# Kernel optimization log

Hardware: AMD Instinct MI355X
Metric: run time of the kernel (lower is better)

The kernel has to match this reference:

```python
import jax, jax.numpy as jnp
from jax import lax
import numpy as np

T, K, KEND = 2048, 4, 8
D, H, WD = 100, 256, 300
V, DICT, C = 20000, 700000, 18


def _build_end_indexed(starts, lens, ids, valid):
    # Group gazetteer words by their END position (the step at which the
    # lattice char cell consumes the word memory cell), padded to KEND slots.
    e_ids = np.zeros((T, KEND), np.int32)
    e_start = np.zeros((T, KEND), np.int32)
    e_mask = np.zeros((T, KEND), np.int32)
    cnt = np.zeros(T, np.int64)
    for t in range(T):
        for k in range(K):
            if valid[t, k]:
                e = int(starts[t, k] + lens[t, k] - 1)
                if cnt[e] < KEND:
                    e_ids[e, cnt[e]] = ids[t, k]
                    e_start[e, cnt[e]] = starts[t, k]
                    e_mask[e, cnt[e]] = 1
                    cnt[e] += 1
    return jnp.asarray(e_ids), jnp.asarray(e_start), jnp.asarray(e_mask)


def setup_inputs():
    ks = jax.random.split(jax.random.key(0), 24)
    inputs = jax.random.randint(ks[0], (1, T), 0, V, dtype=jnp.int32)
    rng = np.random.default_rng(0)
    lens = rng.integers(0, 8, size=(T, K))          # word length; valid iff >= 2
    ids = rng.integers(1, DICT, size=(T, K))        # gazetteer word ids
    pos = np.broadcast_to(np.arange(T)[:, None], (T, K))
    # forward direction: word starts at t, ends at t+len-1
    valid_f = (lens >= 2) & (pos + lens - 1 < T)
    fw_ids, fw_start, fw_mask = _build_end_indexed(pos, lens, ids, valid_f)
    # backward direction, expressed in the flipped frame: start' = T-1-(t+len-1)
    starts_b = T - 1 - (pos + lens - 1)
    valid_b = (lens >= 2) & (starts_b >= 0)
    bw_ids, bw_start, bw_mask = _build_end_indexed(starts_b, lens, ids, valid_b)
    s = 0.08
    nrm = lambda k, shape: jax.random.normal(k, shape, jnp.float32) * s
    p = {}
    i = 1
    for pre in ("fw", "bw"):
        p[pre + "_W_ih"] = nrm(ks[i], (D, 3 * H)); i += 1
        p[pre + "_W_hh"] = nrm(ks[i], (H, 3 * H)); i += 1
        p[pre + "_b"] = jnp.zeros((3 * H,), jnp.float32)
        p[pre + "_aW_ih"] = nrm(ks[i], (D, H)); i += 1
        p[pre + "_aW_hh"] = nrm(ks[i], (H, H)); i += 1
        p[pre + "_ab"] = jnp.zeros((H,), jnp.float32)
        p[pre + "_wW_ih"] = nrm(ks[i], (WD, 3 * H)); i += 1
        p[pre + "_wW_hh"] = nrm(ks[i], (H, 3 * H)); i += 1
        p[pre + "_wb"] = jnp.zeros((3 * H,), jnp.float32)
    out = dict(inputs=inputs, fw_ids=fw_ids, fw_start=fw_start, fw_mask=fw_mask,
               bw_ids=bw_ids, bw_start=bw_start, bw_mask=bw_mask, length=T,
               E=nrm(ks[20], (V, D)), word_table=nrm(ks[21], (DICT, WD)),
               W_lin=nrm(ks[22], (2 * H, C)), b_lin=jnp.zeros((C,), jnp.float32))
    out.update(p)
    return out


def _lattice_pass(x, wemb, start, mask, W_ih, W_hh, b, aW_ih, aW_hh, ab, wW_ih, wW_hh, wb):
    # x: [T,D]; wemb: [T,KEND,WD]; start/mask: [T,KEND]
    Tn, Hn = x.shape[0], W_hh.shape[0]

    def step(carry, xs):
        h, c, Hh, Ch = carry                        # Hh/Ch: [T,H] history of char states
        t, xt, we_t, st, m = xs
        mf = m.astype(x.dtype)[:, None]             # [KEND,1]
        hs, cs = Hh[st], Ch[st]                     # char state at each word's start pos
        # WordLSTMCell: c^w = sigmoid(f)*c_start + sigmoid(i)*tanh(g)
        wi, wf, wg = jnp.split(we_t @ wW_ih + hs @ wW_hh + wb, 3, axis=-1)
        cw = jax.nn.sigmoid(wf) * cs + jax.nn.sigmoid(wi) * jnp.tanh(wg)
        # MultiInputLSTMCell char gates
        ii, oo, gg = jnp.split(xt @ W_ih + h @ W_hh + b, 3, axis=-1)
        i_s, o_s, g_t = jax.nn.sigmoid(ii), jax.nn.sigmoid(oo), jnp.tanh(gg)
        # extra input gate per word, then exp-normalization over {i, alphas}
        alpha = jax.nn.sigmoid(xt @ aW_ih + cw @ aW_hh + ab)   # [KEND,H]
        e_i = jnp.exp(i_s)                                      # [H]
        e_a = jnp.exp(alpha) * mf                               # masked slots drop out
        c_merge = (e_i * g_t + (e_a * cw).sum(0)) / (e_i + e_a.sum(0))
        c_plain = (1.0 - i_s) * c + i_s * g_t                   # no-word branch (f = 1-i)
        c_new = jnp.where(jnp.any(m > 0), c_merge, c_plain)
        h_new = o_s * jnp.tanh(c_new)
        return (h_new, c_new, Hh.at[t].set(h_new), Ch.at[t].set(c_new)), h_new

    z = lambda *sh: jnp.zeros(sh, x.dtype)
    init = (z(Hn), z(Hn), z(Tn, Hn), z(Tn, Hn))
    _, hseq = lax.scan(step, init, (jnp.arange(Tn), x, wemb, start, mask))
    return hseq                                      # [T,H]


def reference(inputs, fw_ids, fw_start, fw_mask, bw_ids, bw_start, bw_mask, length, E,
              word_table, W_lin, b_lin,
              fw_W_ih, fw_W_hh, fw_b, fw_aW_ih, fw_aW_hh, fw_ab, fw_wW_ih, fw_wW_hh, fw_wb,
              bw_W_ih, bw_W_hh, bw_b, bw_aW_ih, bw_aW_hh, bw_ab, bw_wW_ih, bw_wW_hh, bw_wb):
    x = E[inputs[0]]                                 # [T,D] char embeddings (batch=1)
    hf = _lattice_pass(x, word_table[fw_ids], fw_start, fw_mask,
                       fw_W_ih, fw_W_hh, fw_b, fw_aW_ih, fw_aW_hh, fw_ab,
                       fw_wW_ih, fw_wW_hh, fw_wb)
    hb = _lattice_pass(x[::-1], word_table[bw_ids], bw_start, bw_mask,
                       bw_W_ih, bw_W_hh, bw_b, bw_aW_ih, bw_aW_hh, bw_ab,
                       bw_wW_ih, bw_wW_hh, bw_wb)[::-1]
    return (jnp.concatenate([hf, hb], axis=-1) @ W_lin + b_lin)[None]  # [1,T,C]
```

## Files before the change

kernel.cpp:

```cpp
#include <hip/hip_runtime.h>
#include <hip/hip_bf16.h>


#define TSEQ 2048
#define KEND 8
#define DEMB 100
#define H    256
#define H3   768
#define WD   300
#define CCLS 18
#define NTH  256

typedef __attribute__((ext_vector_type(8))) short bf16x8;
typedef __attribute__((ext_vector_type(4))) float f32x4;

#define LO_AT  0
#define LO_A1  131072
#define LO_VS  131584
#define LO_UR  133120
#define LO_RC  143872
#define LO_A2  152064
#define LO_AWS 156288
#define LO_MT  160384
#define SMEM_SCAN 160640

__device__ __forceinline__ float sigf(float x) { return 1.0f / (1.0f + expf(-x)); }
__device__ __forceinline__ float bf2f(unsigned u) { return __uint_as_float(u << 16); }
__device__ __forceinline__ unsigned f2bf(float f) {
  union { float f; unsigned u; } x; x.f = f;
  unsigned r = x.u + 0x7fffu + ((x.u >> 16) & 1u);
  return r >> 16;
}

__global__ __launch_bounds__(64) void k_pack(
    const float* __restrict__ W_hh_f, const float* __restrict__ wW_hh_f, const float* __restrict__ aW_hh_f,
    const float* __restrict__ W_hh_b, const float* __restrict__ wW_hh_b, const float* __restrict__ aW_hh_b,
    unsigned short* __restrict__ Wpk)
{
  const int T = blockIdx.x, dir = blockIdx.y;
  const int lane = threadIdx.x;
  const float* Wg = dir ? W_hh_b  : W_hh_f;
  const float* Ww = dir ? wW_hh_b : wW_hh_f;
  const float* Wa = dir ? aW_hh_b : aW_hh_f;
  for (int ks = 0; ks < 8; ++ks) {
    bf16x8 sv;
#pragma unroll
    for (int e = 0; e < 8; ++e) {
      const int k = ks * 32 + (lane >> 4) * 8 + e;
      float f;
      if (T < 96) {
        const int c = T * 16 + (lane & 15);
        f = (c < H3) ? Wg[(size_t)k * H3 + c] : Ww[(size_t)k * H3 + (c - H3)];
      } else {
        const int c = (T - 96) * 16 + (lane & 15);
        f = Wa[(size_t)k * H + c];
      }
      sv[e] = (short)f2bf(f);
    }
    *(bf16x8*)(Wpk + (((size_t)dir * 112 + T) * 8 + ks) * 512 + lane * 8) = sv;
  }
}

__global__ __launch_bounds__(256) void k_embed(
    const int* __restrict__ inputs, const float* __restrict__ E,
    const float* __restrict__ W_ih_f, const float* __restrict__ b_f,
    const float* __restrict__ aW_ih_f, const float* __restrict__ ab_f,
    const float* __restrict__ W_ih_b, const float* __restrict__ b_b,
    const float* __restrict__ aW_ih_b, const float* __restrict__ ab_b,
    __hip_bfloat16* __restrict__ xg, float* __restrict__ xa)
{
  const int t = blockIdx.x, dir = blockIdx.y;
  const int tid = threadIdx.x;
  const float* W_ih = dir ? W_ih_b : W_ih_f;
  const float* bb   = dir ? b_b    : b_f;
  const float* aW   = dir ? aW_ih_b : aW_ih_f;
  const float* ab   = dir ? ab_b   : ab_f;
  const int src = dir ? (TSEQ - 1 - t) : t;

  __shared__ float xr[DEMB];
  if (tid < DEMB) xr[tid] = E[(size_t)inputs[src] * DEMB + tid];
  __syncthreads();

  float a0 = bb[tid], a1 = bb[H + tid], a2 = bb[2 * H + tid], a3 = ab[tid];
  for (int r = 0; r < DEMB; r += 4) {
    const float4 e4 = *reinterpret_cast<const float4*>(&xr[r]);
    const float ev[4] = {e4.x, e4.y, e4.z, e4.w};
#pragma unroll
    for (int kk = 0; kk < 4; ++kk) {
      const float* wp = W_ih + (size_t)(r + kk) * H3 + tid;
      a0 += ev[kk] * wp[0];
      a1 += ev[kk] * wp[H];
      a2 += ev[kk] * wp[2 * H];
      a3 += ev[kk] * aW[(size_t)(r + kk) * H + tid];
    }
  }
  __hip_bfloat16* xgrow = xg + ((size_t)dir * TSEQ + t) * H3;
  xgrow[tid]         = __float2bfloat16(a0);
  xgrow[H + tid]     = __float2bfloat16(a1);
  xgrow[2 * H + tid] = __float2bfloat16(a2);
  xa[((size_t)dir * TSEQ + t) * H + tid] = a3;
}

__global__ __launch_bounds__(256) void k_wordgates(
    const int* __restrict__ fw_ids, const int* __restrict__ fw_mask,
    const int* __restrict__ bw_ids, const int* __restrict__ bw_mask,
    const float* __restrict__ word_table,
    const float* __restrict__ wW_ih_f, const float* __restrict__ wb_f,
    const float* __restrict__ wW_ih_b, const float* __restrict__ wb_b,
    __hip_bfloat16* __restrict__ wg)
{
  const int t = blockIdx.x, dir = blockIdx.y;
  const int tid = threadIdx.x;
  const int* ids = (dir ? bw_ids : fw_ids) + t * KEND;
  const int* msk = (dir ? bw_mask : fw_mask) + t * KEND;
  const float* wW = dir ? wW_ih_b : wW_ih_f;
  const float* wb = dir ? wb_b    : wb_f;

  __shared__ float we[KEND][WD];
  for (int w = 0; w < KEND; ++w) {
    if (msk[w]) {
      const float* src = word_table + (size_t)ids[w] * WD;
      for (int i = tid; i < WD; i += 256) we[w][i] = src[i];
    }
  }
  __syncthreads();

  __hip_bfloat16* out = wg + ((size_t)dir * TSEQ + t) * KEND * H3;
  for (int w = 0; w < KEND; ++w) {
    if (!msk[w]) continue;
    float a0 = wb[tid], a1 = wb[H + tid], a2 = wb[2 * H + tid];
    for (int r = 0; r < WD; r += 4) {
      const float4 e4 = *reinterpret_cast<const float4*>(&we[w][r]);
      const float ev[4] = {e4.x, e4.y, e4.z, e4.w};
#pragma unroll
      for (int kk = 0; kk < 4; ++kk) {
        const float* wp = wW + (size_t)(r + kk) * H3 + tid;
        a0 += ev[kk] * wp[0];
        a1 += ev[kk] * wp[H];
        a2 += ev[kk] * wp[2 * H];
      }
    }
    out[w * H3 + tid]         = __float2bfloat16(a0);
    out[w * H3 + H + tid]     = __float2bfloat16(a1);
    out[w * H3 + 2 * H + tid] = __float2bfloat16(a2);
  }
}

__global__ __launch_bounds__(NTH, 1) void k_scan(
    const __hip_bfloat16* __restrict__ xg, const float* __restrict__ xa,
    const __hip_bfloat16* __restrict__ wgG, float* __restrict__ hseq,
    const int* __restrict__ fw_start, const int* __restrict__ fw_mask,
    const int* __restrict__ bw_start, const int* __restrict__ bw_mask,
    const unsigned short* __restrict__ Wpk,
    unsigned long long* __restrict__ xb, unsigned* __restrict__ xf)
{
  const int gid = blockIdx.x;
  if (gid != 0 && gid != 1 && gid != 8 && gid != 9) return;
  const int dir  = gid & 1;
  const int side = gid >> 3;

  extern __shared__ char smem[];
  unsigned short* A1_16 = (unsigned short*)(smem + LO_A1);
  unsigned short* vS16  = (unsigned short*)(smem + LO_VS);
  unsigned short* ur16  = (unsigned short*)(smem + LO_UR);
  float* ringC = (float*)(smem + LO_RC);
  unsigned short* awS16 = (unsigned short*)(smem + LO_AWS);
  int* metaI = (int*)(smem + LO_MT);

  const int tid  = threadIdx.x;
  const int lane = tid & 63;
  const int wv   = tid >> 6;
  const int lmod = lane & 15;
  const int lgrp = lane >> 4;

  const int* startA = dir ? bw_start : fw_start;
  const int* maskA  = dir ? bw_mask  : fw_mask;
  const char* WpkD = (const char*)(Wpk + (size_t)dir * 112 * 8 * 512);

  unsigned long long* myPay = xb + (size_t)((dir * 2 + side) * 2) * 192;
  const unsigned long long* peerPay = xb + (size_t)((dir * 2 + (side ^ 1)) * 2) * 192;
  unsigned* myFlag   = xf + (dir * 2 + side) * 32;
  unsigned* peerFlag = xf + (dir * 2 + (side ^ 1)) * 32;

  bf16x8 rW[12][8];
  {
    const char* rp = WpkD + (size_t)(side * 48 + wv * 12) * 8192 + lane * 16;
#pragma unroll
    for (int n = 0; n < 12; ++n)
#pragma unroll
      for (int ks = 0; ks < 8; ++ks)
        rW[n][ks] = *(const bf16x8*)(rp + (n * 8 + ks) * 1024);
  }
  for (int o = tid * 16; o < 131072; o += NTH * 16)
    *(uint4*)(smem + LO_AT + o) = *(const uint4*)(WpkD + (size_t)96 * 8192 + o);
  if (tid < 32) *(uint4*)(smem + LO_A1 + tid * 16) = uint4{0, 0, 0, 0};
  for (int o = tid * 16; o < 4224; o += NTH * 16)
    *(uint4*)(smem + LO_A2 + o) = uint4{0, 0, 0, 0};
  for (int o = tid * 16; o < 8192; o += NTH * 16)
    *(uint4*)(smem + LO_RC + o) = uint4{0, 0, 0, 0};

  unsigned nxI = 0, nxO = 0, nxG = 0; float nxA = 0.f;
  unsigned cxI = 0, cxO = 0, cxG = 0; float cxA = 0.f;
  int nmt = 0;
  {
    const unsigned short* xr = (const unsigned short*)(xg + (size_t)dir * TSEQ * H3);
    nxI = xr[tid]; nxO = xr[H + tid]; nxG = xr[2 * H + tid];
    nxA = xa[(size_t)dir * TSEQ * H + tid];
    if (wv == 3) {
      if (lane < 8) nmt = maskA[lane];
      else if (lane < 16) nmt = startA[lane - 8];
    }
  }
  __syncthreads();
  if (wv == 3) {
    int mAll[8], sAll[8];
#pragma unroll
    for (int s = 0; s < 8; ++s) { mAll[s] = __shfl(nmt, s); sAll[s] = __shfl(nmt, 8 + s); }
    if (lane == 0) {
      int n = 0;
      for (int s = 0; s < 8; ++s)
        if (mAll[s]) { metaI[1 + n] = s; metaI[9 + n] = sAll[s]; ++n; }
      metaI[0] = n;
    }
  }
  cxI = nxI; cxO = nxO; cxG = nxG; cxA = nxA;
  __syncthreads();

  for (int t = 0; t < TSEQ; ++t) {
    const int par = t & 1;
    const int* mp = metaI + par * 32;
    const int nw = mp[0];
    const int us7 = (t + 6) % 7;
    unsigned short* stage16 = side ? (ur16 + us7 * 768) : vS16;
    unsigned short* rcv16   = side ? vS16 : (ur16 + us7 * 768);
    int hasL2w = 0;
    for (int w = 0; w < nw; ++w) hasL2w |= (mp[9 + w] == t - 1);

    unsigned short wgv[24];
#pragma unroll
    for (int it = 0; it < 8; ++it) {
      const int u0 = tid + it * NTH;
      if (u0 < nw * 256) {
        const int w = u0 >> 8, j = u0 & 255;
        const int slot = mp[1 + w];
        const unsigned short* wgp =
            (const unsigned short*)wgG + ((size_t)(dir * TSEQ + t) * KEND + slot) * H3 + j;
        wgv[it * 3 + 0] = wgp[0];
        wgv[it * 3 + 1] = wgp[256];
        wgv[it * 3 + 2] = wgp[512];
      }
    }

#pragma unroll
    for (int g = 0; g < 2; ++g) {
      f32x4 acc[6];
#pragma unroll
      for (int n = 0; n < 6; ++n) acc[n] = f32x4{0.f, 0.f, 0.f, 0.f};
#pragma unroll
      for (int ks = 0; ks < 8; ++ks) {
        const bf16x8 av = *(const bf16x8*)(smem + LO_A1 + ks * 64 + lgrp * 16);
#pragma unroll
        for (int n = 0; n < 6; ++n)
          acc[n] = __builtin_amdgcn_mfma_f32_16x16x32_bf16(av, rW[g * 6 + n][ks], acc[n], 0, 0, 0);
      }
      if (lane < 16) {
#pragma unroll
        for (int n = 0; n < 6; ++n)
          stage16[(wv * 12 + g * 6 + n) * 16 + lane] = (unsigned short)f2bf(acc[n][0]);
      }
    }
    __syncthreads();

    if (tid < 192) {
      const unsigned long long q = *(const unsigned long long*)((const char*)stage16 + tid * 8);
      __hip_atomic_store(myPay + par * 192 + tid, q, __ATOMIC_RELAXED, __HIP_MEMORY_SCOPE_AGENT);
    }
    __syncthreads();

    if (tid == 0)
      __hip_atomic_store(myFlag, (unsigned)(t + 1), __ATOMIC_RELAXED, __HIP_MEMORY_SCOPE_AGENT);

    {
      const int tn = (t + 1 < TSEQ) ? t + 1 : TSEQ - 1;
      const unsigned short* xr = (const unsigned short*)(xg + ((size_t)dir * TSEQ + tn) * H3);
      nxI = xr[tid]; nxO = xr[H + tid]; nxG = xr[2 * H + tid];
      nxA = xa[((size_t)dir * TSEQ + tn) * H + tid];
      if (wv == 3) {
        if (lane < 8) nmt = maskA[tn * KEND + lane];
        else if (lane < 16) nmt = startA[tn * KEND + (lane - 8)];
      }
    }
#pragma unroll
    for (int it = 0; it < 8; ++it) {
      const int u0 = tid + it * NTH;
      if (u0 < nw * 256) {
        const int w = u0 >> 8, j = u0 & 255;
        const int s = mp[9 + w];
        if (side == 1 || s != t - 1) {
          const unsigned short* ur = ur16 + (s % 7) * 768;
          const float wi  = bf2f(wgv[it * 3 + 0]) + bf2f(ur[j]);
          const float wf  = bf2f(wgv[it * 3 + 1]) + bf2f(ur[256 + j]);
          const float wgg = bf2f(wgv[it * 3 + 2]) + bf2f(ur[512 + j]);
          const float cs  = ringC[(s & 7) * 256 + j];
          const float cv  = sigf(wf) * cs + sigf(wi) * tanhf(wgg);
          *(unsigned short*)(smem + LO_A2 + w * 528 + j * 2) = (unsigned short)f2bf(cv);
        }
      }
    }

    if (tid == 0) {
      while (__hip_atomic_load(peerFlag, __ATOMIC_RELAXED, __HIP_MEMORY_SCOPE_AGENT) < (unsigned)(t + 1))
        __builtin_amdgcn_s_sleep(1);
    }
    __syncthreads();

    if (tid < 192) {
      const unsigned long long q =
          __hip_atomic_load(peerPay + par * 192 + tid, __ATOMIC_RELAXED, __HIP_MEMORY_SCOPE_AGENT);
      *(unsigned long long*)((char*)rcv16 + tid * 8) = q;
    }
    __syncthreads();

    if (hasL2w) {
      if (side == 0) {
#pragma unroll
        for (int it = 0; it < 8; ++it) {
          const int u0 = tid + it * NTH;
          if (u0 < nw * 256) {
            const int w = u0 >> 8, j = u0 & 255;
            const int s = mp[9 + w];
            if (s == t - 1) {
              const unsigned short* ur = ur16 + (s % 7) * 768;
              const float wi  = bf2f(wgv[it * 3 + 0]) + bf2f(ur[j]);
              const float wf  = bf2f(wgv[it * 3 + 1]) + bf2f(ur[256 + j]);
              const float wgg = bf2f(wgv[it * 3 + 2]) + bf2f(ur[512 + j]);
              const float cs  = ringC[(s & 7) * 256 + j];
              const float cv  = sigf(wf) * cs + sigf(wi) * tanhf(wgg);
              *(unsigned short*)(smem + LO_A2 + w * 528 + j * 2) = (unsigned short)f2bf(cv);
            }
          }
        }
      }
      __syncthreads();
    }

    if (nw > 0) {
      const int r2 = (lmod > 7) ? 7 : lmod;
      f32x4 ac[4];
#pragma unroll
      for (int m = 0; m < 4; ++m) ac[m] = f32x4{0.f, 0.f, 0.f, 0.f};
#pragma unroll
      for (int ks = 0; ks < 8; ++ks) {
        const bf16x8 a2v = *(const bf16x8*)(smem + LO_A2 + r2 * 528 + ks * 64 + lgrp * 16);
#pragma unroll
        for (int m = 0; m < 4; ++m) {
          const bf16x8 b = *(const bf16x8*)(smem + LO_AT + (size_t)(wv * 4 + m) * 8192 + ks * 1024 + lane * 16);
          ac[m] = __builtin_amdgcn_mfma_f32_16x16x32_bf16(a2v, b, ac[m], 0, 0, 0);
        }
      }
#pragma unroll
      for (int m = 0; m < 4; ++m) {
#pragma unroll
        for (int r = 0; r < 4; ++r) {
          const int row = lgrp * 4 + r;
          if (row < nw) awS16[row * 256 + (wv * 4 + m) * 16 + lmod] = (unsigned short)f2bf(ac[m][r]);
        }
      }
    }
    __syncthreads();

    {
      const int j = tid;
      const float i_s = sigf(bf2f(cxI) + bf2f(vS16[j]));
      const float o_s = sigf(bf2f(cxO) + bf2f(vS16[256 + j]));
      const float g_t = tanhf(bf2f(cxG) + bf2f(vS16[512 + j]));
      float cnew;
      if (nw > 0) {
        const float e_i = expf(i_s);
        float num = e_i * g_t, den = e_i;
        for (int w = 0; w < nw; ++w) {
          const float a  = sigf(cxA + bf2f(awS16[w * 256 + j]));
          const float ea = expf(a);
          num += ea * bf2f(*(const unsigned short*)(smem + LO_A2 + w * 528 + j * 2));
          den += ea;
        }
        cnew = num / den;
      } else {
        cnew = (1.f - i_s) * ringC[((t - 1) & 7) * 256 + j] + i_s * g_t;
      }
      const float hnew = o_s * tanhf(cnew);
      ringC[(t & 7) * 256 + j] = cnew;
      A1_16[j] = (unsigned short)f2bf(hnew);
      if ((side == 0) == (j < 128))
        hseq[((size_t)dir * TSEQ + t) * H + j] = hnew;
    }
    if (wv == 3) {
      int mAll[8], sAll[8];
#pragma unroll
      for (int s = 0; s < 8; ++s) { mAll[s] = __shfl(nmt, s); sAll[s] = __shfl(nmt, 8 + s); }
      if (lane == 0) {
        int* mq = metaI + ((t + 1) & 1) * 32;
        int n = 0;
        for (int s = 0; s < 8; ++s)
          if (mAll[s]) { mq[1 + n] = s; mq[9 + n] = sAll[s]; ++n; }
        mq[0] = n;
      }
    }
    cxI = nxI; cxO = nxO; cxG = nxG; cxA = nxA;
    __syncthreads();
  }
}

__global__ __launch_bounds__(64) void k_proj(
    const float* __restrict__ hseq, const float* __restrict__ W_lin,
    const float* __restrict__ b_lin, float* __restrict__ out)
{
  const int t = blockIdx.x;
  const int tid = threadIdx.x;
  __shared__ float hrow[2 * H];
  for (int i = tid; i < H; i += 64) {
    hrow[i]     = hseq[(size_t)t * H + i];
    hrow[H + i] = hseq[((size_t)TSEQ + (TSEQ - 1 - t)) * H + i];
  }
  __syncthreads();
  if (tid < CCLS) {
    float acc = b_lin[tid];
    for (int j = 0; j < 2 * H; ++j) acc += hrow[j] * W_lin[(size_t)j * CCLS + tid];
    out[(size_t)t * CCLS + tid] = acc;
  }
}

extern "C" void kernel_launch(void* const* d_in, const int* in_sizes, int n_in,
                              void* d_out, int out_size, void* d_ws, size_t ws_size,
                              hipStream_t stream)
{
  const int* inputs   = (const int*)d_in[0];
  const int* fw_ids   = (const int*)d_in[1];
  const int* fw_start = (const int*)d_in[2];
  const int* fw_mask  = (const int*)d_in[3];
  const int* bw_ids   = (const int*)d_in[4];
  const int* bw_start = (const int*)d_in[5];
  const int* bw_mask  = (const int*)d_in[6];
  const float* E          = (const float*)d_in[8];
  const float* word_table = (const float*)d_in[9];
  const float* W_lin      = (const float*)d_in[10];
  const float* b_lin      = (const float*)d_in[11];
  const float* fw_W_ih  = (const float*)d_in[12];
  const float* fw_W_hh  = (const float*)d_in[13];
  const float* fw_b     = (const float*)d_in[14];
  const float* fw_aW_ih = (const float*)d_in[15];
  const float* fw_aW_hh = (const float*)d_in[16];
  const float* fw_ab    = (const float*)d_in[17];
  const float* fw_wW_ih = (const float*)d_in[18];
  const float* fw_wW_hh = (const float*)d_in[19];
  const float* fw_wb    = (const float*)d_in[20];
  const float* bw_W_ih  = (const float*)d_in[21];
  const float* bw_W_hh  = (const float*)d_in[22];
  const float* bw_b     = (const float*)d_in[23];
  const float* bw_aW_ih = (const float*)d_in[24];
  const float* bw_aW_hh = (const float*)d_in[25];
  const float* bw_ab    = (const float*)d_in[26];
  const float* bw_wW_ih = (const float*)d_in[27];
  const float* bw_wW_hh = (const float*)d_in[28];
  const float* bw_wb    = (const float*)d_in[29];

  char* p = (char*)d_ws;
  __hip_bfloat16* xg = (__hip_bfloat16*)p;  p += (size_t)2 * TSEQ * H3 * 2;
  float* xa   = (float*)p;                  p += (size_t)2 * TSEQ * H * 4;
  float* hseq = (float*)p;                  p += (size_t)2 * TSEQ * H * 4;
  __hip_bfloat16* wg = (__hip_bfloat16*)p;  p += (size_t)2 * TSEQ * KEND * H3 * 2;
  unsigned short* Wpk = (unsigned short*)p; p += (size_t)2 * 112 * 8 * 512 * 2;
  unsigned long long* xb = (unsigned long long*)p; p += (size_t)2 * 2 * 2 * 192 * 8;
  unsigned* xf = (unsigned*)p;              p += 512;

  hipFuncSetAttribute((const void*)k_scan,
                      hipFuncAttributeMaxDynamicSharedMemorySize, SMEM_SCAN);
  hipMemsetAsync(xf, 0, 512, stream);

  k_pack<<<dim3(112, 2), 64, 0, stream>>>(
      fw_W_hh, fw_wW_hh, fw_aW_hh, bw_W_hh, bw_wW_hh, bw_aW_hh, Wpk);
  k_embed<<<dim3(TSEQ, 2), 256, 0, stream>>>(
      inputs, E, fw_W_ih, fw_b, fw_aW_ih, fw_ab, bw_W_ih, bw_b, bw_aW_ih, bw_ab, xg, xa);
  k_wordgates<<<dim3(TSEQ, 2), 256, 0, stream>>>(
      fw_ids, fw_mask, bw_ids, bw_mask, word_table, fw_wW_ih, fw_wb, bw_wW_ih, bw_wb, wg);
  k_scan<<<16, NTH, SMEM_SCAN, stream>>>(
      xg, xa, wg, hseq, fw_start, fw_mask, bw_start, bw_mask, Wpk, xb, xf);
  k_proj<<<TSEQ, 64, 0, stream>>>(hseq, W_lin, b_lin, (float*)d_out);
}
```

Baseline: 14.28 ms.

## Make side-1 block a pipelined word-recurrence helper with tagged h/u exchange

Previously two blocks per direction did a symmetric step: each computed half the gates, exchanged payloads and waited on a flag every step. Now side 0 computes all char-cell gates locally. Side 1 only waits for h, computes the word-cell recurrent product, and publishes it as timestamp-tagged 64-bit words, so no separate flag is needed. Side 0 reads the word product lazily with a lag of two steps, and waits for the previous step's product only when a word starting at t-1 is present. This takes the peer round trip off the critical path at most steps, but spinning on tagged loads adds polling traffic.

```diff
diff --git a/kernel.cpp b/kernel.cpp
--- a/kernel.cpp
+++ b/kernel.cpp
@@ -16,13 +16,13 @@
 
 #define LO_AT  0
 #define LO_A1  131072
-#define LO_VS  131584
-#define LO_UR  133120
-#define LO_RC  143872
-#define LO_A2  152064
-#define LO_AWS 156288
-#define LO_MT  160384
-#define SMEM_SCAN 160640
+#define LO_UR  131584
+#define LO_RC  142336
+#define LO_PRE 150528
+#define LO_A2  153600
+#define LO_AWS 157824
+#define LO_MT  161920
+#define SMEM_SCAN 162176
 
 __device__ __forceinline__ float sigf(float x) { return 1.0f / (1.0f + expf(-x)); }
 __device__ __forceinline__ float bf2f(unsigned u) { return __uint_as_float(u << 16); }
@@ -152,7 +152,7 @@
     const int* __restrict__ fw_start, const int* __restrict__ fw_mask,
     const int* __restrict__ bw_start, const int* __restrict__ bw_mask,
     const unsigned short* __restrict__ Wpk,
-    unsigned long long* __restrict__ xb, unsigned* __restrict__ xf)
+    unsigned long long* __restrict__ hx, unsigned long long* __restrict__ ux)
 {
   const int gid = blockIdx.x;
   if (gid != 0 && gid != 1 && gid != 8 && gid != 9) return;
@@ -161,9 +161,9 @@
 
   extern __shared__ char smem[];
   unsigned short* A1_16 = (unsigned short*)(smem + LO_A1);
-  unsigned short* vS16  = (unsigned short*)(smem + LO_VS);
   unsigned short* ur16  = (unsigned short*)(smem + LO_UR);
   float* ringC = (float*)(smem + LO_RC);
+  float* preS  = (float*)(smem + LO_PRE);
   unsigned short* awS16 = (unsigned short*)(smem + LO_AWS);
   int* metaI = (int*)(smem + LO_MT);
 
@@ -173,14 +173,10 @@
   const int lmod = lane & 15;
   const int lgrp = lane >> 4;
 
-  const int* startA = dir ? bw_start : fw_start;
-  const int* maskA  = dir ? bw_mask  : fw_mask;
   const char* WpkD = (const char*)(Wpk + (size_t)dir * 112 * 8 * 512);
 
-  unsigned long long* myPay = xb + (size_t)((dir * 2 + side) * 2) * 192;
-  const unsigned long long* peerPay = xb + (size_t)((dir * 2 + (side ^ 1)) * 2) * 192;
-  unsigned* myFlag   = xf + (dir * 2 + side) * 32;
-  unsigned* peerFlag = xf + (dir * 2 + (side ^ 1)) * 32;
+  unsigned long long* hbuf = hx + (size_t)dir * 2 * 128;
+  unsigned long long* ubuf = ux + (size_t)dir * 2 * 384;
 
   bf16x8 rW[12][8];
   {
@@ -191,6 +187,51 @@
       for (int ks = 0; ks < 8; ++ks)
         rW[n][ks] = *(const bf16x8*)(rp + (n * 8 + ks) * 1024);
   }
+
+  if (side == 1) {
+    __syncthreads();
+    for (int t = 1; t < TSEQ; ++t) {
+      if (tid < 128) {
+        const unsigned long long* src = hbuf + (size_t)((t - 1) & 1) * 128;
+        unsigned long long q;
+        do { q = __hip_atomic_load(src + tid, __ATOMIC_RELAXED, __HIP_MEMORY_SCOPE_AGENT); }
+        while ((unsigned)(q >> 32) != (unsigned)t);
+        *(unsigned*)((char*)A1_16 + tid * 4) = (unsigned)q;
+      }
+      __syncthreads();
+#pragma unroll
+      for (int g = 0; g < 2; ++g) {
+        f32x4 acc[6];
+#pragma unroll
+        for (int n = 0; n < 6; ++n) acc[n] = f32x4{0.f, 0.f, 0.f, 0.f};
+#pragma unroll
+        for (int ks = 0; ks < 8; ++ks) {
+          const bf16x8 av = *(const bf16x8*)(smem + LO_A1 + ks * 64 + lgrp * 16);
+#pragma unroll
+          for (int n = 0; n < 6; ++n)
+            acc[n] = __builtin_amdgcn_mfma_f32_16x16x32_bf16(av, rW[g * 6 + n][ks], acc[n], 0, 0, 0);
+        }
+#pragma unroll
+        for (int n = 0; n < 6; ++n) {
+          const unsigned hb = f2bf(acc[n][0]) & 0xffffu;
+          const unsigned ob = (unsigned)__shfl_down((int)hb, 1) & 0xffffu;
+          if (lane < 16 && !(lane & 1)) {
+            const int tix = wv * 12 + g * 6 + n;
+            const unsigned long long q =
+                ((unsigned long long)(unsigned)t << 32) | (hb | (ob << 16));
+            __hip_atomic_store(ubuf + (size_t)((t - 1) & 1) * 384 + tix * 8 + (lane >> 1), q,
+                               __ATOMIC_RELAXED, __HIP_MEMORY_SCOPE_AGENT);
+          }
+        }
+      }
+      __syncthreads();
+    }
+    return;
+  }
+
+  const int* startA = dir ? bw_start : fw_start;
+  const int* maskA  = dir ? bw_mask  : fw_mask;
+
   for (int o = tid * 16; o < 131072; o += NTH * 16)
     *(uint4*)(smem + LO_AT + o) = *(const uint4*)(WpkD + (size_t)96 * 8192 + o);
   if (tid < 32) *(uint4*)(smem + LO_A1 + tid * 16) = uint4{0, 0, 0, 0};
@@ -226,13 +267,12 @@
   cxI = nxI; cxO = nxO; cxG = nxG; cxA = nxA;
   __syncthreads();
 
+  int uHave = -1;
+
   for (int t = 0; t < TSEQ; ++t) {
     const int par = t & 1;
     const int* mp = metaI + par * 32;
     const int nw = mp[0];
-    const int us7 = (t + 6) % 7;
-    unsigned short* stage16 = side ? (ur16 + us7 * 768) : vS16;
-    unsigned short* rcv16   = side ? vS16 : (ur16 + us7 * 768);
     int hasL2w = 0;
     for (int w = 0; w < nw; ++w) hasL2w |= (mp[9 + w] == t - 1);
 
@@ -266,19 +306,24 @@
       if (lane < 16) {
 #pragma unroll
         for (int n = 0; n < 6; ++n)
-          stage16[(wv * 12 + g * 6 + n) * 16 + lane] = (unsigned short)f2bf(acc[n][0]);
-      }
-    }
-    __syncthreads();
-
-    if (tid < 192) {
-      const unsigned long long q = *(const unsigned long long*)((const char*)stage16 + tid * 8);
-      __hip_atomic_store(myPay + par * 192 + tid, q, __ATOMIC_RELAXED, __HIP_MEMORY_SCOPE_AGENT);
-    }
-    __syncthreads();
-
-    if (tid == 0)
-      __hip_atomic_store(myFlag, (unsigned)(t + 1), __ATOMIC_RELAXED, __HIP_MEMORY_SCOPE_AGENT);
+          preS[(wv * 12 + g * 6 + n) * 16 + lane] = acc[n][0];
+      }
+    }
+
+    if (t >= 2 && uHave < t - 2) {
+      const int s = t - 2;
+      const unsigned long long* src = ubuf + (size_t)(s & 1) * 384;
+      unsigned long long q;
+      do { q = __hip_atomic_load(src + tid, __ATOMIC_RELAXED, __HIP_MEMORY_SCOPE_AGENT); }
+      while ((unsigned)(q >> 32) != (unsigned)(s + 1));
+      *(unsigned*)((char*)ur16 + (s % 7) * 1536 + tid * 4) = (unsigned)q;
+      if (tid < 128) {
+        do { q = __hip_atomic_load(src + 256 + tid, __ATOMIC_RELAXED, __HIP_MEMORY_SCOPE_AGENT); }
+        while ((unsigned)(q >> 32) != (unsigned)(s + 1));
+        *(unsigned*)((char*)ur16 + (s % 7) * 1536 + (256 + tid) * 4) = (unsigned)q;
+      }
+      uHave = t - 2;
+    }
 
     {
       const int tn = (t + 1 < TSEQ) ? t + 1 : TSEQ - 1;
@@ -290,13 +335,15 @@
         else if (lane < 16) nmt = startA[tn * KEND + (lane - 8)];
       }
     }
+    __syncthreads();
+
 #pragma unroll
     for (int it = 0; it < 8; ++it) {
       const int u0 = tid + it * NTH;
       if (u0 < nw * 256) {
         const int w = u0 >> 8, j = u0 & 255;
         const int s = mp[9 + w];
-        if (side == 1 || s != t - 1) {
+        if (s != t - 1) {
           const unsigned short* ur = ur16 + (s % 7) * 768;
           const float wi  = bf2f(wgv[it * 3 + 0]) + bf2f(ur[j]);
           const float wf  = bf2f(wgv[it * 3 + 1]) + bf2f(ur[256 + j]);
@@ -307,42 +354,41 @@
         }
       }
     }
-
-    if (tid == 0) {
-      while (__hip_atomic_load(peerFlag, __ATOMIC_RELAXED, __HIP_MEMORY_SCOPE_AGENT) < (unsigned)(t + 1))
-        __builtin_amdgcn_s_sleep(1);
+    if (hasL2w) {
+      {
+        const int s = t - 1;
+        const unsigned long long* src = ubuf + (size_t)(s & 1) * 384;
+        unsigned long long q;
+        do { q = __hip_atomic_load(src + tid, __ATOMIC_RELAXED, __HIP_MEMORY_SCOPE_AGENT); }
+        while ((unsigned)(q >> 32) != (unsigned)(s + 1));
+        *(unsigned*)((char*)ur16 + (s % 7) * 1536 + tid * 4) = (unsigned)q;
+        if (tid < 128) {
+          do { q = __hip_atomic_load(src + 256 + tid, __ATOMIC_RELAXED, __HIP_MEMORY_SCOPE_AGENT); }
+          while ((unsigned)(q >> 32) != (unsigned)(s + 1));
+          *(unsigned*)((char*)ur16 + (s % 7) * 1536 + (256 + tid) * 4) = (unsigned)q;
+        }
+        uHave = t - 1;
+      }
+      __syncthreads();
+#pragma unroll
+      for (int it = 0; it < 8; ++it) {
+        const int u0 = tid + it * NTH;
+        if (u0 < nw * 256) {
+          const int w = u0 >> 8, j = u0 & 255;
+          const int s = mp[9 + w];
+          if (s == t - 1) {
+            const unsigned short* ur = ur16 + (s % 7) * 768;
+            const float wi  = bf2f(wgv[it * 3 + 0]) + bf2f(ur[j]);
+            const float wf  = bf2f(wgv[it * 3 + 1]) + bf2f(ur[256 + j]);
+            const float wgg = bf2f(wgv[it * 3 + 2]) + bf2f(ur[512 + j]);
+            const float cs  = ringC[(s & 7) * 256 + j];
+            const float cv  = sigf(wf) * cs + sigf(wi) * tanhf(wgg);
+            *(unsigned short*)(smem + LO_A2 + w * 528 + j * 2) = (unsigned short)f2bf(cv);
+          }
+        }
+      }
     }
     __syncthreads();
-
-    if (tid < 192) {
-      const unsigned long long q =
-          __hip_atomic_load(peerPay + par * 192 + tid, __ATOMIC_RELAXED, __HIP_MEMORY_SCOPE_AGENT);
-      *(unsigned long long*)((char*)rcv16 + tid * 8) = q;
-    }
-    __syncthreads();
-
-    if (hasL2w) {
-      if (side == 0) {
-#pragma unroll
-        for (int it = 0; it < 8; ++it) {
-          const int u0 = tid + it * NTH;
-          if (u0 < nw * 256) {
-            const int w = u0 >> 8, j = u0 & 255;
-            const int s = mp[9 + w];
-            if (s == t - 1) {
-              const unsigned short* ur = ur16 + (s % 7) * 768;
-              const float wi  = bf2f(wgv[it * 3 + 0]) + bf2f(ur[j]);
-              const float wf  = bf2f(wgv[it * 3 + 1]) + bf2f(ur[256 + j]);
-              const float wgg = bf2f(wgv[it * 3 + 2]) + bf2f(ur[512 + j]);
-              const float cs  = ringC[(s & 7) * 256 + j];
-              const float cv  = sigf(wf) * cs + sigf(wi) * tanhf(wgg);
-              *(unsigned short*)(smem + LO_A2 + w * 528 + j * 2) = (unsigned short)f2bf(cv);
-            }
-          }
-        }
-      }
-      __syncthreads();
-    }
 
     if (nw > 0) {
       const int r2 = (lmod > 7) ? 7 : lmod;
@@ -371,9 +417,9 @@
 
     {
       const int j = tid;
-      const float i_s = sigf(bf2f(cxI) + bf2f(vS16[j]));
-      const float o_s = sigf(bf2f(cxO) + bf2f(vS16[256 + j]));
-      const float g_t = tanhf(bf2f(cxG) + bf2f(vS16[512 + j]));
+      const float i_s = sigf(bf2f(cxI) + preS[j]);
+      const float o_s = sigf(bf2f(cxO) + preS[256 + j]);
+      const float g_t = tanhf(bf2f(cxG) + preS[512 + j]);
       float cnew;
       if (nw > 0) {
         const float e_i = expf(i_s);
@@ -390,9 +436,16 @@
       }
       const float hnew = o_s * tanhf(cnew);
       ringC[(t & 7) * 256 + j] = cnew;
-      A1_16[j] = (unsigned short)f2bf(hnew);
-      if ((side == 0) == (j < 128))
-        hseq[((size_t)dir * TSEQ + t) * H + j] = hnew;
+      const unsigned hb = f2bf(hnew) & 0xffffu;
+      A1_16[j] = (unsigned short)hb;
+      hseq[((size_t)dir * TSEQ + t) * H + j] = hnew;
+      const unsigned ob = (unsigned)__shfl_xor((int)hb, 1) & 0xffffu;
+      if (!(tid & 1)) {
+        const unsigned long long q =
+            ((unsigned long long)(unsigned)(t + 1) << 32) | (hb | (ob << 16));
+        __hip_atomic_store(hbuf + (size_t)par * 128 + (tid >> 1), q,
+                           __ATOMIC_RELAXED, __HIP_MEMORY_SCOPE_AGENT);
+      }
     }
     if (wv == 3) {
       int mAll[8], sAll[8];
@@ -470,12 +523,12 @@
   float* hseq = (float*)p;                  p += (size_t)2 * TSEQ * H * 4;
   __hip_bfloat16* wg = (__hip_bfloat16*)p;  p += (size_t)2 * TSEQ * KEND * H3 * 2;
   unsigned short* Wpk = (unsigned short*)p; p += (size_t)2 * 112 * 8 * 512 * 2;
-  unsigned long long* xb = (unsigned long long*)p; p += (size_t)2 * 2 * 2 * 192 * 8;
-  unsigned* xf = (unsigned*)p;              p += 512;
+  unsigned long long* hx = (unsigned long long*)p; p += (size_t)2 * 2 * 128 * 8;
+  unsigned long long* ux = (unsigned long long*)p; p += (size_t)2 * 2 * 384 * 8;
 
   hipFuncSetAttribute((const void*)k_scan,
                       hipFuncAttributeMaxDynamicSharedMemorySize, SMEM_SCAN);
-  hipMemsetAsync(xf, 0, 512, stream);
+  hipMemsetAsync(hx, 0, (size_t)2 * 2 * 128 * 8 + (size_t)2 * 2 * 384 * 8, stream);
 
   k_pack<<<dim3(112, 2), 64, 0, stream>>>(
       fw_W_hh, fw_wW_hh, fw_aW_hh, bw_W_hh, bw_wW_hh, bw_aW_hh, Wpk);
@@ -484,6 +537,6 @@
   k_wordgates<<<dim3(TSEQ, 2), 256, 0, stream>>>(
       fw_ids, fw_mask, bw_ids, bw_mask, word_table, fw_wW_ih, fw_wb, bw_wW_ih, bw_wb, wg);
   k_scan<<<16, NTH, SMEM_SCAN, stream>>>(
-      xg, xa, wg, hseq, fw_start, fw_mask, bw_start, bw_mask, Wpk, xb, xf);
+      xg, xa, wg, hseq, fw_start, fw_mask, bw_start, bw_mask, Wpk, hx, ux);
   k_proj<<<TSEQ, 64, 0, stream>>>(hseq, W_lin, b_lin, (float*)d_out);
 }
```

Result: slower. 16.33 ms (+14.4%).

## Decouple cross-block exchange and defer word-cell payload waits in lattice scan

Applied to the files above, without the earlier changes.

The symmetric per-step handshake between the two blocks of each direction becomes asymmetric. Side 0 now publishes the char-gate matvec and side 1 waits for it only right before the cell update. Side 1's word-gate payload is consumed lazily by side 0: immediately only when a word started at the previous step, otherwise prefetched at the end of the step. Payload packing moves into registers via lane shuffles with direct atomic stores, which removes two block barriers per step. This is meant to shorten the serial per-step critical path, but the flag and slot parity logic is more delicate and could race or deadlock if wrong.

```diff
diff --git a/kernel.cpp b/kernel.cpp
--- a/kernel.cpp
+++ b/kernel.cpp
@@ -152,7 +152,8 @@
     const int* __restrict__ fw_start, const int* __restrict__ fw_mask,
     const int* __restrict__ bw_start, const int* __restrict__ bw_mask,
     const unsigned short* __restrict__ Wpk,
-    unsigned long long* __restrict__ xb, unsigned* __restrict__ xf)
+    unsigned long long* __restrict__ vb, unsigned long long* __restrict__ ub,
+    unsigned* __restrict__ xf)
 {
   const int gid = blockIdx.x;
   if (gid != 0 && gid != 1 && gid != 8 && gid != 9) return;
@@ -177,10 +178,11 @@
   const int* maskA  = dir ? bw_mask  : fw_mask;
   const char* WpkD = (const char*)(Wpk + (size_t)dir * 112 * 8 * 512);
 
-  unsigned long long* myPay = xb + (size_t)((dir * 2 + side) * 2) * 192;
-  const unsigned long long* peerPay = xb + (size_t)((dir * 2 + (side ^ 1)) * 2) * 192;
-  unsigned* myFlag   = xf + (dir * 2 + side) * 32;
-  unsigned* peerFlag = xf + (dir * 2 + (side ^ 1)) * 32;
+  unsigned long long* myPay = (side ? ub : vb) + (size_t)dir * 2 * 192;
+  const unsigned long long* ubuf = ub + (size_t)dir * 2 * 192;
+  const unsigned long long* vbuf = vb + (size_t)dir * 2 * 192;
+  unsigned* vFlag = xf + dir * 64;
+  unsigned* uFlag = xf + dir * 64 + 32;
 
   bf16x8 rW[12][8];
   {
@@ -226,13 +228,16 @@
   cxI = nxI; cxO = nxO; cxG = nxG; cxA = nxA;
   __syncthreads();
 
+  int uHave = -1, pfValid = 0, pfS = 0;
+  unsigned long long pq = 0;
+
   for (int t = 0; t < TSEQ; ++t) {
     const int par = t & 1;
     const int* mp = metaI + par * 32;
     const int nw = mp[0];
     const int us7 = (t + 6) % 7;
     unsigned short* stage16 = side ? (ur16 + us7 * 768) : vS16;
-    unsigned short* rcv16   = side ? vS16 : (ur16 + us7 * 768);
+    const int pubSlot = side ? (par ^ 1) : par;
     int hasL2w = 0;
     for (int w = 0; w < nw; ++w) hasL2w |= (mp[9 + w] == t - 1);
 
@@ -263,22 +268,32 @@
         for (int n = 0; n < 6; ++n)
           acc[n] = __builtin_amdgcn_mfma_f32_16x16x32_bf16(av, rW[g * 6 + n][ks], acc[n], 0, 0, 0);
       }
-      if (lane < 16) {
-#pragma unroll
-        for (int n = 0; n < 6; ++n)
-          stage16[(wv * 12 + g * 6 + n) * 16 + lane] = (unsigned short)f2bf(acc[n][0]);
-      }
-    }
-    __syncthreads();
-
-    if (tid < 192) {
-      const unsigned long long q = *(const unsigned long long*)((const char*)stage16 + tid * 8);
-      __hip_atomic_store(myPay + par * 192 + tid, q, __ATOMIC_RELAXED, __HIP_MEMORY_SCOPE_AGENT);
-    }
-    __syncthreads();
-
-    if (tid == 0)
-      __hip_atomic_store(myFlag, (unsigned)(t + 1), __ATOMIC_RELAXED, __HIP_MEMORY_SCOPE_AGENT);
+#pragma unroll
+      for (int n = 0; n < 6; ++n) {
+        const unsigned hb = f2bf(acc[n][0]) & 0xffffu;
+        const unsigned v1 = (unsigned)__shfl_down((int)hb, 1) & 0xffffu;
+        const unsigned v2 = (unsigned)__shfl_down((int)hb, 2) & 0xffffu;
+        const unsigned v3 = (unsigned)__shfl_down((int)hb, 3) & 0xffffu;
+        if (lane < 16) {
+          const int tix = wv * 12 + g * 6 + n;
+          stage16[tix * 16 + lane] = (unsigned short)hb;
+          if ((lane & 3) == 0) {
+            const unsigned long long q =
+                (unsigned long long)(hb | (v1 << 16)) |
+                ((unsigned long long)(v2 | (v3 << 16)) << 32);
+            __hip_atomic_store(myPay + (size_t)pubSlot * 192 + tix * 4 + (lane >> 2), q,
+                               __ATOMIC_RELAXED, __HIP_MEMORY_SCOPE_AGENT);
+          }
+        }
+      }
+    }
+
+    if (side == 0 && pfValid) {
+      if (tid < 192)
+        *(unsigned long long*)((char*)ur16 + (pfS % 7) * 1536 + tid * 8) = pq;
+      uHave = pfS;
+      pfValid = 0;
+    }
 
     {
       const int tn = (t + 1 < TSEQ) ? t + 1 : TSEQ - 1;
@@ -290,6 +305,13 @@
         else if (lane < 16) nmt = startA[tn * KEND + (lane - 8)];
       }
     }
+    __syncthreads();
+
+    if (tid == 0) {
+      if (side) __hip_atomic_store(uFlag, (unsigned)t, __ATOMIC_RELAXED, __HIP_MEMORY_SCOPE_AGENT);
+      else      __hip_atomic_store(vFlag, (unsigned)(t + 1), __ATOMIC_RELAXED, __HIP_MEMORY_SCOPE_AGENT);
+    }
+
 #pragma unroll
     for (int it = 0; it < 8; ++it) {
       const int u0 = tid + it * NTH;
@@ -308,66 +330,82 @@
       }
     }
 
-    if (tid == 0) {
-      while (__hip_atomic_load(peerFlag, __ATOMIC_RELAXED, __HIP_MEMORY_SCOPE_AGENT) < (unsigned)(t + 1))
-        __builtin_amdgcn_s_sleep(1);
-    }
-    __syncthreads();
-
-    if (tid < 192) {
-      const unsigned long long q =
-          __hip_atomic_load(peerPay + par * 192 + tid, __ATOMIC_RELAXED, __HIP_MEMORY_SCOPE_AGENT);
-      *(unsigned long long*)((char*)rcv16 + tid * 8) = q;
-    }
-    __syncthreads();
-
-    if (hasL2w) {
-      if (side == 0) {
-#pragma unroll
-        for (int it = 0; it < 8; ++it) {
-          const int u0 = tid + it * NTH;
-          if (u0 < nw * 256) {
-            const int w = u0 >> 8, j = u0 & 255;
-            const int s = mp[9 + w];
-            if (s == t - 1) {
-              const unsigned short* ur = ur16 + (s % 7) * 768;
-              const float wi  = bf2f(wgv[it * 3 + 0]) + bf2f(ur[j]);
-              const float wf  = bf2f(wgv[it * 3 + 1]) + bf2f(ur[256 + j]);
-              const float wgg = bf2f(wgv[it * 3 + 2]) + bf2f(ur[512 + j]);
-              const float cs  = ringC[(s & 7) * 256 + j];
-              const float cv  = sigf(wf) * cs + sigf(wi) * tanhf(wgg);
-              *(unsigned short*)(smem + LO_A2 + w * 528 + j * 2) = (unsigned short)f2bf(cv);
-            }
+    if (side == 0 && hasL2w) {
+      if (tid == 0) {
+        while (__hip_atomic_load(uFlag, __ATOMIC_RELAXED, __HIP_MEMORY_SCOPE_AGENT) < (unsigned)t)
+          __builtin_amdgcn_s_sleep(1);
+      }
+      __syncthreads();
+      if (tid < 192) {
+        const unsigned long long q =
+            __hip_atomic_load(ubuf + (size_t)((t - 1) & 1) * 192 + tid,
+                              __ATOMIC_RELAXED, __HIP_MEMORY_SCOPE_AGENT);
+        *(unsigned long long*)((char*)ur16 + ((t - 1) % 7) * 1536 + tid * 8) = q;
+      }
+      uHave = t - 1;
+      __syncthreads();
+#pragma unroll
+      for (int it = 0; it < 8; ++it) {
+        const int u0 = tid + it * NTH;
+        if (u0 < nw * 256) {
+          const int w = u0 >> 8, j = u0 & 255;
+          const int s = mp[9 + w];
+          if (s == t - 1) {
+            const unsigned short* ur = ur16 + (s % 7) * 768;
+            const float wi  = bf2f(wgv[it * 3 + 0]) + bf2f(ur[j]);
+            const float wf  = bf2f(wgv[it * 3 + 1]) + bf2f(ur[256 + j]);
+            const float wgg = bf2f(wgv[it * 3 + 2]) + bf2f(ur[512 + j]);
+            const float cs  = ringC[(s & 7) * 256 + j];
+            const float cv  = sigf(wf) * cs + sigf(wi) * tanhf(wgg);
+            *(unsigned short*)(smem + LO_A2 + w * 528 + j * 2) = (unsigned short)f2bf(cv);
           }
         }
       }
-      __syncthreads();
     }
 
     if (nw > 0) {
-      const int r2 = (lmod > 7) ? 7 : lmod;
-      f32x4 ac[4];
-#pragma unroll
-      for (int m = 0; m < 4; ++m) ac[m] = f32x4{0.f, 0.f, 0.f, 0.f};
-#pragma unroll
-      for (int ks = 0; ks < 8; ++ks) {
-        const bf16x8 a2v = *(const bf16x8*)(smem + LO_A2 + r2 * 528 + ks * 64 + lgrp * 16);
+      __syncthreads();
+
+      {
+        const int r2 = (lmod > 7) ? 7 : lmod;
+        f32x4 ac[4];
+#pragma unroll
+        for (int m = 0; m < 4; ++m) ac[m] = f32x4{0.f, 0.f, 0.f, 0.f};
+#pragma unroll
+        for (int ks = 0; ks < 8; ++ks) {
+          const bf16x8 a2v = *(const bf16x8*)(smem + LO_A2 + r2 * 528 + ks * 64 + lgrp * 16);
+#pragma unroll
+          for (int m = 0; m < 4; ++m) {
+            const bf16x8 b = *(const bf16x8*)(smem + LO_AT + (size_t)(wv * 4 + m) * 8192 + ks * 1024 + lane * 16);
+            ac[m] = __builtin_amdgcn_mfma_f32_16x16x32_bf16(a2v, b, ac[m], 0, 0, 0);
+          }
+        }
 #pragma unroll
         for (int m = 0; m < 4; ++m) {
-          const bf16x8 b = *(const bf16x8*)(smem + LO_AT + (size_t)(wv * 4 + m) * 8192 + ks * 1024 + lane * 16);
-          ac[m] = __builtin_amdgcn_mfma_f32_16x16x32_bf16(a2v, b, ac[m], 0, 0, 0);
+#pragma unroll
+          for (int r = 0; r < 4; ++r) {
+            const int row = lgrp * 4 + r;
+            if (row < nw) awS16[row * 256 + (wv * 4 + m) * 16 + lmod] = (unsigned short)f2bf(ac[m][r]);
+          }
         }
       }
-#pragma unroll
-      for (int m = 0; m < 4; ++m) {
-#pragma unroll
-        for (int r = 0; r < 4; ++r) {
-          const int row = lgrp * 4 + r;
-          if (row < nw) awS16[row * 256 + (wv * 4 + m) * 16 + lmod] = (unsigned short)f2bf(ac[m][r]);
-        }
-      }
-    }
-    __syncthreads();
+      __syncthreads();
+    }
+
+    if (side == 1) {
+      if (tid == 0) {
+        while (__hip_atomic_load(vFlag, __ATOMIC_RELAXED, __HIP_MEMORY_SCOPE_AGENT) < (unsigned)(t + 1))
+          __builtin_amdgcn_s_sleep(1);
+      }
+      __syncthreads();
+      if (tid < 192) {
+        const unsigned long long q =
+            __hip_atomic_load(vbuf + (size_t)par * 192 + tid,
+                              __ATOMIC_RELAXED, __HIP_MEMORY_SCOPE_AGENT);
+        *(unsigned long long*)((char*)vS16 + tid * 8) = q;
+      }
+      __syncthreads();
+    }
 
     {
       const int j = tid;
@@ -407,7 +445,20 @@
       }
     }
     cxI = nxI; cxO = nxO; cxG = nxG; cxA = nxA;
-    __syncthreads();
+
+    if (side == 0 && t >= 1 && t + 1 < TSEQ && uHave < t - 1) {
+      if (tid == 0) {
+        while (__hip_atomic_load(uFlag, __ATOMIC_RELAXED, __HIP_MEMORY_SCOPE_AGENT) < (unsigned)t)
+          __builtin_amdgcn_s_sleep(1);
+      }
+      __syncthreads();
+      if (tid < 192)
+        pq = __hip_atomic_load(ubuf + (size_t)((t - 1) & 1) * 192 + tid,
+                               __ATOMIC_RELAXED, __HIP_MEMORY_SCOPE_AGENT);
+      pfS = t - 1; pfValid = 1;
+    } else {
+      __syncthreads();
+    }
   }
 }
 
@@ -470,7 +521,8 @@
   float* hseq = (float*)p;                  p += (size_t)2 * TSEQ * H * 4;
   __hip_bfloat16* wg = (__hip_bfloat16*)p;  p += (size_t)2 * TSEQ * KEND * H3 * 2;
   unsigned short* Wpk = (unsigned short*)p; p += (size_t)2 * 112 * 8 * 512 * 2;
-  unsigned long long* xb = (unsigned long long*)p; p += (size_t)2 * 2 * 2 * 192 * 8;
+  unsigned long long* vb = (unsigned long long*)p; p += (size_t)2 * 2 * 192 * 8;
+  unsigned long long* ub = (unsigned long long*)p; p += (size_t)2 * 2 * 192 * 8;
   unsigned* xf = (unsigned*)p;              p += 512;
 
   hipFuncSetAttribute((const void*)k_scan,
@@ -484,6 +536,6 @@
   k_wordgates<<<dim3(TSEQ, 2), 256, 0, stream>>>(
       fw_ids, fw_mask, bw_ids, bw_mask, word_table, fw_wW_ih, fw_wb, bw_wW_ih, bw_wb, wg);
   k_scan<<<16, NTH, SMEM_SCAN, stream>>>(
-      xg, xa, wg, hseq, fw_start, fw_mask, bw_start, bw_mask, Wpk, xb, xf);
+      xg, xa, wg, hseq, fw_start, fw_mask, bw_start, bw_mask, Wpk, vb, ub, xf);
   k_proj<<<TSEQ, 64, 0, stream>>>(hseq, W_lin, b_lin, (float*)d_out);
 }
```

Result: slower. 20.10 ms (+40.8%).
